# Kernel tuning notes

Measured on AMD Instinct MI355X. Metric: run time of the kernel, lower is better.

## Reference

```python
import jax, jax.numpy as jnp
import numpy as np

B, Y = 1024, 50000
MAX_TRIALS = 4096


def setup_inputs() -> dict:
    key = jax.random.key(0)
    k1, k2 = jax.random.split(key)
    input_ = jax.random.normal(k1, (B, Y), dtype=jnp.float32)
    pos = jax.random.randint(k2, (B,), 0, Y)
    target = jnp.zeros((B, Y), jnp.float32).at[jnp.arange(B), pos].set(1.0)
    return {"input_": input_, "target": target, "max_num_trials": MAX_TRIALS}


def reference(input_, target, max_num_trials):
    """WARP loss. The torch original sequentially samples negatives WITHOUT
    replacement per row until margin 1 + s_neg - s_pos >= 0 or max_num_trials
    is hit. Sampling without replacement == taking a uniform random
    permutation of the negative labels and scanning it; the first violating
    position t gives num_trials = t+1. This lets us fully vectorize the
    irregular loop while computing identical math (up to RNG stream)."""
    Bn, Yn = input_.shape
    rows = jnp.arange(Bn)
    pos = jnp.argmax(target, axis=1)                 # one positive per row (as J[i,1])
    pos_score = input_[rows, pos]                    # [B]

    # uniform random permutation of the Y-1 negatives per row:
    # random sort keys, force the positive label to sort last, drop it.
    u = jax.random.uniform(jax.random.key(42), (Bn, Yn))
    u = u.at[rows, pos].set(2.0)
    perm = jnp.argsort(u, axis=1)[:, : Yn - 1]       # [B, Y-1] negative label ids

    neg_scores = jnp.take_along_axis(input_, perm, axis=1)   # [B, Y-1]
    margins = 1.0 + neg_scores - pos_score[:, None]
    trial_ok = jnp.arange(Yn - 1)[None, :] < max_num_trials
    viol = (margins >= 0.0) & trial_ok
    found = jnp.any(viol, axis=1)
    first = jnp.argmax(viol, axis=1)                 # first violating trial index
    num_trials = (first + 1).astype(jnp.float32)
    # loss_weight = log(floor((Y-1)/num_trials)); 0 when no violator found
    L = jnp.where(found, jnp.log(jnp.floor((Yn - 1.0) / num_trials)), 0.0)
    neg_score = jnp.where(
        found, jnp.take_along_axis(neg_scores, first[:, None], axis=1)[:, 0], 0.0
    )
    loss = L * (1.0 - pos_score + neg_score)         # [B]
    return jnp.sum(loss, keepdims=True)              # shape (1,), as torch.sum(dim=0, keepdim=True)
```

## Files before the change

### kernel.cpp

```cpp
#include <hip/hip_runtime.h>
#include <stdint.h>

#define BN 1024
#define YN 50000
#define SEGS 8
#define SEGLEN 6250
#define CAP 192
#define KEYHI_T (1u << 14)

#define TF_ROUND(r) { x0 += x1; x1 = (x1 << (r)) | (x1 >> (32 - (r))); x1 ^= x0; }

__device__ __forceinline__ uint32_t tf_bits(uint32_t ctr) {
    const uint32_t ks0 = 0u;
    const uint32_t ks1 = 42u;
    const uint32_t ks2 = 0x1BD11BDAu ^ 0u ^ 42u;
    uint32_t x0 = ks0;
    uint32_t x1 = ctr + ks1;
    TF_ROUND(13) TF_ROUND(15) TF_ROUND(26) TF_ROUND(6)
    x0 += ks1; x1 += ks2 + 1u;
    TF_ROUND(17) TF_ROUND(29) TF_ROUND(16) TF_ROUND(24)
    x0 += ks2; x1 += ks0 + 2u;
    TF_ROUND(13) TF_ROUND(15) TF_ROUND(26) TF_ROUND(6)
    x0 += ks0; x1 += ks1 + 3u;
    TF_ROUND(17) TF_ROUND(29) TF_ROUND(16) TF_ROUND(24)
    x0 += ks1; x1 += ks2 + 4u;
    TF_ROUND(13) TF_ROUND(15) TF_ROUND(26) TF_ROUND(6)
    x0 += ks2; x1 += ks0 + 5u;
    return x0 ^ x1;
}

struct WS {
    uint32_t* cnt; int* flag; int* pos; float* ps; float* row_loss; uint32_t* cand;
};
static inline WS ws_layout(void* d_ws) {
    uint32_t* p = (uint32_t*)d_ws;
    WS w;
    w.cnt = p; w.flag = (int*)(p + BN); w.pos = (int*)(p + 2 * BN);
    w.ps = (float*)(p + 3 * BN); w.row_loss = (float*)(p + 4 * BN);
    w.cand = p + 5 * BN;
    return w;
}

__global__ __launch_bounds__(256) void gen_kernel(
    const float* __restrict__ input, const float* __restrict__ target,
    uint32_t* __restrict__ cnt, uint32_t* __restrict__ cand,
    int* __restrict__ pos_out, float* __restrict__ ps_out)
{
    const int tid = threadIdx.x;
    if (blockIdx.x < BN) {
        const int row = blockIdx.x;
        const size_t base = (size_t)row * YN;
        __shared__ volatile int s_pos;
        if (tid == 0) s_pos = -1;
        __syncthreads();
        const float4* t4 = (const float4*)(target + base);
        for (int j4 = tid; j4 < YN / 4; j4 += 256) {
            if (s_pos >= 0) break;
            float4 v = t4[j4];
            int c0 = 4 * j4;
            if (v.x != 0.0f) s_pos = c0;
            if (v.y != 0.0f) s_pos = c0 + 1;
            if (v.z != 0.0f) s_pos = c0 + 2;
            if (v.w != 0.0f) s_pos = c0 + 3;
        }
        __syncthreads();
        if (tid == 0) {
            int p = s_pos;
            pos_out[row] = p;
            ps_out[row] = input[base + p];
        }
        return;
    }
    const int b = blockIdx.x - BN;
    const int row = b >> 3;
    const int seg = b & 7;
    const uint32_t base32 = (uint32_t)row * YN;
    const int start = seg * SEGLEN;
    const int end = start + SEGLEN;
    uint32_t* mycnt = cnt + row;
    uint32_t* mycand = cand + row * CAP;
    for (int col = start + tid; col < end; col += 256) {
        uint32_t bits = tf_bits(base32 + (uint32_t)col);
        uint32_t kh = bits >> 9;
        if (kh < KEYHI_T) {
            uint32_t idx = atomicAdd(mycnt, 1u);
            if (idx < CAP) mycand[idx] = (kh << 17) | (uint32_t)col;
        }
    }
}

__global__ __launch_bounds__(256) void resolve_kernel(
    const float* __restrict__ input, const uint32_t* __restrict__ cnt,
    const uint32_t* __restrict__ cand, const int* __restrict__ pos_,
    const float* __restrict__ ps_, const int* __restrict__ mt_ptr,
    float* __restrict__ row_loss, int* __restrict__ flag)
{
    const int gtid = blockIdx.x * 256 + threadIdx.x;
    const int row = gtid >> 6;
    const int lane = gtid & 63;
    const uint32_t n = cnt[row];
    if (n > CAP) { if (lane == 0) flag[row] = 1; return; }
    const int pos = pos_[row];
    const float ps = ps_[row];
    const uint32_t* cl = cand + row * CAP;
    const float* rowp = input + (size_t)row * YN;

    uint32_t mk = 0xFFFFFFFFu;
    for (uint32_t i = lane; i < n; i += 64) {
        uint32_t e = cl[i];
        int col = (int)(e & 0x1FFFFu);
        if (col == pos) continue;
        float s = rowp[col];
        if ((1.0f + s) - ps >= 0.0f) mk = (e < mk) ? e : mk;
    }
    for (int off = 32; off > 0; off >>= 1) {
        uint32_t o = (uint32_t)__shfl_xor((int)mk, off, 64);
        mk = (o < mk) ? o : mk;
    }
    if (mk == 0xFFFFFFFFu) {
        if (lane == 0) flag[row] = 1;
        return;
    }
    uint32_t c = 0;
    for (uint32_t i = lane; i < n; i += 64) {
        uint32_t e = cl[i];
        int col = (int)(e & 0x1FFFFu);
        c += ((e < mk) && (col != pos)) ? 1u : 0u;
    }
    for (int off = 32; off > 0; off >>= 1) c += (uint32_t)__shfl_xor((int)c, off, 64);
    if (lane == 0) {
        uint32_t rank = c;
        float loss = 0.0f;
        if (rank < (uint32_t)mt_ptr[0]) {
            int cstar = (int)(mk & 0x1FFFFu);
            float ns = rowp[cstar];
            float nt = (float)(rank + 1u);
            loss = logf(floorf(49999.0f / nt)) * ((1.0f - ps) + ns);
        }
        row_loss[row] = loss;
    }
}

__global__ __launch_bounds__(256) void fallback_kernel(
    const float* __restrict__ input, const int* __restrict__ flag,
    const int* __restrict__ pos_, const float* __restrict__ ps_,
    const int* __restrict__ mt_ptr, float* __restrict__ row_loss)
{
    const int row = blockIdx.x;
    if (!flag[row]) return;
    const int tid = threadIdx.x;
    const int pos = pos_[row];
    const float ps = ps_[row];
    const uint32_t base32 = (uint32_t)row * YN;
    const float* rowp = input + (size_t)row * YN;

    __shared__ uint64_t smin[256];
    __shared__ uint32_t ssum[256];

    uint64_t mk = ~0ull;
    for (int col = tid; col < YN; col += 256) {
        uint32_t bits = tf_bits(base32 + (uint32_t)col);
        uint64_t key = ((uint64_t)(bits >> 9) << 17) | (uint32_t)col;
        float m = (1.0f + rowp[col]) - ps;
        if ((m >= 0.0f) && (col != pos) && (key < mk)) mk = key;
    }
    smin[tid] = mk;
    __syncthreads();
    for (int s = 128; s > 0; s >>= 1) {
        if (tid < s) { uint64_t o = smin[tid + s]; if (o < smin[tid]) smin[tid] = o; }
        __syncthreads();
    }
    const uint64_t kstar = smin[0];
    if (kstar == ~0ull) {
        if (tid == 0) row_loss[row] = 0.0f;
        return;
    }
    uint32_t c = 0;
    for (int col = tid; col < YN; col += 256) {
        uint32_t bits = tf_bits(base32 + (uint32_t)col);
        uint64_t key = ((uint64_t)(bits >> 9) << 17) | (uint32_t)col;
        c += ((key < kstar) && (col != pos)) ? 1u : 0u;
    }
    ssum[tid] = c;
    __syncthreads();
    for (int s = 128; s > 0; s >>= 1) {
        if (tid < s) ssum[tid] += ssum[tid + s];
        __syncthreads();
    }
    if (tid == 0) {
        uint32_t rank = ssum[0];
        float loss = 0.0f;
        if (rank < (uint32_t)mt_ptr[0]) {
            int cstar = (int)(kstar & 0x1FFFFull);
            float ns = rowp[cstar];
            float nt = (float)(rank + 1u);
            loss = logf(floorf(49999.0f / nt)) * ((1.0f - ps) + ns);
        }
        row_loss[row] = loss;
    }
}

__global__ __launch_bounds__(256) void reduce_kernel(
    const float* __restrict__ row_loss, float* __restrict__ out)
{
    __shared__ float s[256];
    int tid = threadIdx.x;
    float acc = 0.0f;
    for (int i = tid; i < BN; i += 256) acc += row_loss[i];
    s[tid] = acc;
    __syncthreads();
    for (int st = 128; st > 0; st >>= 1) {
        if (tid < st) s[tid] += s[tid + st];
        __syncthreads();
    }
    if (tid == 0) out[0] = s[0];
}

extern "C" void kernel_launch(void* const* d_in, const int* in_sizes, int n_in,
                              void* d_out, int out_size, void* d_ws, size_t ws_size,
                              hipStream_t stream) {
    const float* input  = (const float*)d_in[0];
    const float* target = (const float*)d_in[1];
    const int*   mt     = (const int*)d_in[2];
    float* out = (float*)d_out;
    WS w = ws_layout(d_ws);

    hipMemsetAsync(d_ws, 0, 2 * BN * sizeof(uint32_t), stream);

    gen_kernel<<<BN + BN * SEGS, 256, 0, stream>>>(
        input, target, w.cnt, w.cand, w.pos, w.ps);
    resolve_kernel<<<BN / 4, 256, 0, stream>>>(
        input, w.cnt, w.cand, w.pos, w.ps, mt, w.row_loss, w.flag);
    fallback_kernel<<<BN, 256, 0, stream>>>(
        input, w.flag, w.pos, w.ps, mt, w.row_loss);
    reduce_kernel<<<1, 256, 0, stream>>>(w.row_loss, out);
}
```

Before: 457.0 us.

## Use per-segment LDS candidate counters, 4-wide Threefry, lower key threshold

Candidate collection now counts in shared memory per segment block and writes one per-segment count, so the global atomics and the workspace memset go away. Threefry is computed four counters at a time using the alignbit rotate, which adds instruction-level parallelism. The key threshold is halved so each segment holds at most 32 candidates, and resolve reads a fixed 256 slots held in registers. The risk is that more rows find no violator among the smaller candidate set or overflow a segment, which sends them to the expensive fallback scan.

```diff
diff --git a/kernel.cpp b/kernel.cpp
--- a/kernel.cpp
+++ b/kernel.cpp
@@ -5,45 +5,73 @@
 #define YN 50000
 #define SEGS 8
 #define SEGLEN 6250
-#define CAP 192
-#define KEYHI_T (1u << 14)
-
-#define TF_ROUND(r) { x0 += x1; x1 = (x1 << (r)) | (x1 >> (32 - (r))); x1 ^= x0; }
+#define SEGCAP 32
+#define KEYHI_T (1u << 13)
+
+#define ROTL(x, r) __builtin_amdgcn_alignbit((x), (x), 32u - (r))
+#define TF4(r) { \
+    x0[0] += x1[0]; x0[1] += x1[1]; x0[2] += x1[2]; x0[3] += x1[3]; \
+    x1[0] = ROTL(x1[0], r); x1[1] = ROTL(x1[1], r); \
+    x1[2] = ROTL(x1[2], r); x1[3] = ROTL(x1[3], r); \
+    x1[0] ^= x0[0]; x1[1] ^= x0[1]; x1[2] ^= x0[2]; x1[3] ^= x0[3]; }
+#define INJ4(a, b) { \
+    x0[0] += (a); x0[1] += (a); x0[2] += (a); x0[3] += (a); \
+    x1[0] += (b); x1[1] += (b); x1[2] += (b); x1[3] += (b); }
+
+__device__ __forceinline__ void tf_bits4(uint32_t ctr0, uint32_t out[4]) {
+    const uint32_t ks0 = 0u, ks1 = 42u, ks2 = 0x1BD11BDAu ^ 0u ^ 42u;
+    uint32_t x0[4], x1[4];
+#pragma unroll
+    for (int k = 0; k < 4; ++k) { x0[k] = ks0; x1[k] = ctr0 + (uint32_t)k + ks1; }
+    TF4(13) TF4(15) TF4(26) TF4(6)
+    INJ4(ks1, ks2 + 1u)
+    TF4(17) TF4(29) TF4(16) TF4(24)
+    INJ4(ks2, ks0 + 2u)
+    TF4(13) TF4(15) TF4(26) TF4(6)
+    INJ4(ks0, ks1 + 3u)
+    TF4(17) TF4(29) TF4(16) TF4(24)
+    INJ4(ks1, ks2 + 4u)
+    TF4(13) TF4(15) TF4(26) TF4(6)
+    INJ4(ks2, ks0 + 5u)
+#pragma unroll
+    for (int k = 0; k < 4; ++k) out[k] = x0[k] ^ x1[k];
+}
 
 __device__ __forceinline__ uint32_t tf_bits(uint32_t ctr) {
-    const uint32_t ks0 = 0u;
-    const uint32_t ks1 = 42u;
-    const uint32_t ks2 = 0x1BD11BDAu ^ 0u ^ 42u;
-    uint32_t x0 = ks0;
-    uint32_t x1 = ctr + ks1;
-    TF_ROUND(13) TF_ROUND(15) TF_ROUND(26) TF_ROUND(6)
+    const uint32_t ks0 = 0u, ks1 = 42u, ks2 = 0x1BD11BDAu ^ 0u ^ 42u;
+    uint32_t x0 = ks0, x1 = ctr + ks1;
+#define TFR(r) { x0 += x1; x1 = ROTL(x1, r); x1 ^= x0; }
+    TFR(13) TFR(15) TFR(26) TFR(6)
     x0 += ks1; x1 += ks2 + 1u;
-    TF_ROUND(17) TF_ROUND(29) TF_ROUND(16) TF_ROUND(24)
+    TFR(17) TFR(29) TFR(16) TFR(24)
     x0 += ks2; x1 += ks0 + 2u;
-    TF_ROUND(13) TF_ROUND(15) TF_ROUND(26) TF_ROUND(6)
+    TFR(13) TFR(15) TFR(26) TFR(6)
     x0 += ks0; x1 += ks1 + 3u;
-    TF_ROUND(17) TF_ROUND(29) TF_ROUND(16) TF_ROUND(24)
+    TFR(17) TFR(29) TFR(16) TFR(24)
     x0 += ks1; x1 += ks2 + 4u;
-    TF_ROUND(13) TF_ROUND(15) TF_ROUND(26) TF_ROUND(6)
+    TFR(13) TFR(15) TFR(26) TFR(6)
     x0 += ks2; x1 += ks0 + 5u;
     return x0 ^ x1;
 }
 
 struct WS {
-    uint32_t* cnt; int* flag; int* pos; float* ps; float* row_loss; uint32_t* cand;
+    uint32_t* cnt_seg; int* pos; float* ps; float* row_loss; int* flag; uint32_t* cand;
 };
 static inline WS ws_layout(void* d_ws) {
     uint32_t* p = (uint32_t*)d_ws;
     WS w;
-    w.cnt = p; w.flag = (int*)(p + BN); w.pos = (int*)(p + 2 * BN);
-    w.ps = (float*)(p + 3 * BN); w.row_loss = (float*)(p + 4 * BN);
-    w.cand = p + 5 * BN;
+    w.cnt_seg = p;
+    w.pos = (int*)(p + SEGS * BN);
+    w.ps = (float*)(p + (SEGS + 1) * BN);
+    w.row_loss = (float*)(p + (SEGS + 2) * BN);
+    w.flag = (int*)(p + (SEGS + 3) * BN);
+    w.cand = p + (SEGS + 4) * BN;
     return w;
 }
 
 __global__ __launch_bounds__(256) void gen_kernel(
     const float* __restrict__ input, const float* __restrict__ target,
-    uint32_t* __restrict__ cnt, uint32_t* __restrict__ cand,
+    uint32_t* __restrict__ cnt_seg, uint32_t* __restrict__ cand,
     int* __restrict__ pos_out, float* __restrict__ ps_out)
 {
     const int tid = threadIdx.x;
@@ -74,23 +102,32 @@
     const int b = blockIdx.x - BN;
     const int row = b >> 3;
     const int seg = b & 7;
-    const uint32_t base32 = (uint32_t)row * YN;
+    const uint32_t rowbase = (uint32_t)row * (uint32_t)YN;
     const int start = seg * SEGLEN;
     const int end = start + SEGLEN;
-    uint32_t* mycnt = cnt + row;
-    uint32_t* mycand = cand + row * CAP;
-    for (int col = start + tid; col < end; col += 256) {
-        uint32_t bits = tf_bits(base32 + (uint32_t)col);
-        uint32_t kh = bits >> 9;
-        if (kh < KEYHI_T) {
-            uint32_t idx = atomicAdd(mycnt, 1u);
-            if (idx < CAP) mycand[idx] = (kh << 17) | (uint32_t)col;
-        }
-    }
+    __shared__ uint32_t lcnt;
+    if (tid == 0) lcnt = 0;
+    __syncthreads();
+    uint32_t* mycand = cand + (size_t)(row * SEGS + seg) * SEGCAP;
+    for (int col0 = start + tid * 4; col0 < end; col0 += 1024) {
+        uint32_t o[4];
+        tf_bits4(rowbase + (uint32_t)col0, o);
+#pragma unroll
+        for (int k = 0; k < 4; ++k) {
+            uint32_t kh = o[k] >> 9;
+            int col = col0 + k;
+            if (kh < KEYHI_T && col < end) {
+                uint32_t idx = atomicAdd(&lcnt, 1u);
+                if (idx < SEGCAP) mycand[idx] = (kh << 17) | (uint32_t)col;
+            }
+        }
+    }
+    __syncthreads();
+    if (tid == 0) cnt_seg[row * SEGS + seg] = lcnt;
 }
 
 __global__ __launch_bounds__(256) void resolve_kernel(
-    const float* __restrict__ input, const uint32_t* __restrict__ cnt,
+    const float* __restrict__ input, const uint32_t* __restrict__ cnt_seg,
     const uint32_t* __restrict__ cand, const int* __restrict__ pos_,
     const float* __restrict__ ps_, const int* __restrict__ mt_ptr,
     float* __restrict__ row_loss, int* __restrict__ flag)
@@ -98,20 +135,34 @@
     const int gtid = blockIdx.x * 256 + threadIdx.x;
     const int row = gtid >> 6;
     const int lane = gtid & 63;
-    const uint32_t n = cnt[row];
-    if (n > CAP) { if (lane == 0) flag[row] = 1; return; }
+    const uint32_t* cs = cnt_seg + row * SEGS;
+    uint32_t csl[SEGS];
+    bool over = false;
+#pragma unroll
+    for (int s = 0; s < SEGS; ++s) { csl[s] = cs[s]; over |= (csl[s] > SEGCAP); }
+    if (over) { if (lane == 0) flag[row] = 1; return; }
+
     const int pos = pos_[row];
     const float ps = ps_[row];
-    const uint32_t* cl = cand + row * CAP;
+    const uint32_t* cl = cand + (size_t)row * SEGS * SEGCAP;
     const float* rowp = input + (size_t)row * YN;
 
+    uint32_t ecache[4]; bool vcache[4];
     uint32_t mk = 0xFFFFFFFFu;
-    for (uint32_t i = lane; i < n; i += 64) {
-        uint32_t e = cl[i];
-        int col = (int)(e & 0x1FFFFu);
-        if (col == pos) continue;
-        float s = rowp[col];
-        if ((1.0f + s) - ps >= 0.0f) mk = (e < mk) ? e : mk;
+#pragma unroll
+    for (int it = 0; it < 4; ++it) {
+        int slot = lane + 64 * it;
+        int s = slot >> 5, idx = slot & 31;
+        bool valid = (uint32_t)idx < csl[s];
+        uint32_t e = valid ? cl[slot] : 0xFFFFFFFFu;
+        ecache[it] = e; vcache[it] = valid;
+        if (valid) {
+            int col = (int)(e & 0x1FFFFu);
+            if (col != pos) {
+                float sc = rowp[col];
+                if ((1.0f + sc) - ps >= 0.0f && e < mk) mk = e;
+            }
+        }
     }
     for (int off = 32; off > 0; off >>= 1) {
         uint32_t o = (uint32_t)__shfl_xor((int)mk, off, 64);
@@ -122,13 +173,15 @@
         return;
     }
     uint32_t c = 0;
-    for (uint32_t i = lane; i < n; i += 64) {
-        uint32_t e = cl[i];
+#pragma unroll
+    for (int it = 0; it < 4; ++it) {
+        uint32_t e = ecache[it];
         int col = (int)(e & 0x1FFFFu);
-        c += ((e < mk) && (col != pos)) ? 1u : 0u;
+        c += (vcache[it] && (e < mk) && (col != pos)) ? 1u : 0u;
     }
     for (int off = 32; off > 0; off >>= 1) c += (uint32_t)__shfl_xor((int)c, off, 64);
     if (lane == 0) {
+        flag[row] = 0;
         uint32_t rank = c;
         float loss = 0.0f;
         if (rank < (uint32_t)mt_ptr[0]) {
@@ -151,7 +204,7 @@
     const int tid = threadIdx.x;
     const int pos = pos_[row];
     const float ps = ps_[row];
-    const uint32_t base32 = (uint32_t)row * YN;
+    const uint32_t base32 = (uint32_t)row * (uint32_t)YN;
     const float* rowp = input + (size_t)row * YN;
 
     __shared__ uint64_t smin[256];
@@ -225,12 +278,10 @@
     float* out = (float*)d_out;
     WS w = ws_layout(d_ws);
 
-    hipMemsetAsync(d_ws, 0, 2 * BN * sizeof(uint32_t), stream);
-
     gen_kernel<<<BN + BN * SEGS, 256, 0, stream>>>(
-        input, target, w.cnt, w.cand, w.pos, w.ps);
+        input, target, w.cnt_seg, w.cand, w.pos, w.ps);
     resolve_kernel<<<BN / 4, 256, 0, stream>>>(
-        input, w.cnt, w.cand, w.pos, w.ps, mt, w.row_loss, w.flag);
+        input, w.cnt_seg, w.cand, w.pos, w.ps, mt, w.row_loss, w.flag);
     fallback_kernel<<<BN, 256, 0, stream>>>(
         input, w.flag, w.pos, w.ps, mt, w.row_loss);
     reduce_kernel<<<1, 256, 0, stream>>>(w.row_loss, out);
```

Result: slower. 548.2 us (+20.0%).

## Interleave four Threefry hashes per thread over flattened index space

Applied to the files above, without the earlier changes.

The candidate generation pass now walks the flattened B*Y counter space with a grid-stride loop. Each thread evaluates four Threefry streams interleaved, using alignbit rotates, and folds the zero key-schedule additions away. The candidate threshold and capacity are halved, and the resolve kernel loads at most two candidates per lane without loops and clears the fallback flag itself, so the memset shrinks. This aims to cut ALU and issue cost in the hash-dominated pass. In exchange it computes per-element row/col by division, and the smaller candidate set slightly raises the chance of the slow fallback path.

```diff
diff --git a/kernel.cpp b/kernel.cpp
--- a/kernel.cpp
+++ b/kernel.cpp
@@ -3,45 +3,49 @@
 
 #define BN 1024
 #define YN 50000
-#define SEGS 8
-#define SEGLEN 6250
-#define CAP 192
-#define KEYHI_T (1u << 14)
-
-#define TF_ROUND(r) { x0 += x1; x1 = (x1 << (r)) | (x1 >> (32 - (r))); x1 ^= x0; }
+#define NTOT (BN * YN)
+#define NGROUPS (NTOT / 4)
+#define CAP 96
+#define BITS_T (1u << 22)
+#define HASH_BLOCKS 4096
+#define STRIDE (HASH_BLOCKS * 256)
+
+#define ROTL(x, r) __builtin_amdgcn_alignbit((x), (x), 32u - (r))
+#define RND(b, a, r) { b += a; a = ROTL(a, r); a ^= b; }
+#define RND4(r) { RND(b0,a0,r) RND(b1,a1,r) RND(b2,a2,r) RND(b3,a3,r) }
+#define INJ4(db, da) { b0 += (db); b1 += (db); b2 += (db); b3 += (db); \
+                       a0 += (da); a1 += (da); a2 += (da); a3 += (da); }
 
 __device__ __forceinline__ uint32_t tf_bits(uint32_t ctr) {
-    const uint32_t ks0 = 0u;
-    const uint32_t ks1 = 42u;
-    const uint32_t ks2 = 0x1BD11BDAu ^ 0u ^ 42u;
-    uint32_t x0 = ks0;
-    uint32_t x1 = ctr + ks1;
-    TF_ROUND(13) TF_ROUND(15) TF_ROUND(26) TF_ROUND(6)
+    const uint32_t ks1 = 42u, ks2 = 0x1BD11BF0u;
+    uint32_t x0 = 0u, x1 = ctr + ks1;
+#define TFR(r) { x0 += x1; x1 = ROTL(x1, r); x1 ^= x0; }
+    TFR(13) TFR(15) TFR(26) TFR(6)
     x0 += ks1; x1 += ks2 + 1u;
-    TF_ROUND(17) TF_ROUND(29) TF_ROUND(16) TF_ROUND(24)
-    x0 += ks2; x1 += ks0 + 2u;
-    TF_ROUND(13) TF_ROUND(15) TF_ROUND(26) TF_ROUND(6)
-    x0 += ks0; x1 += ks1 + 3u;
-    TF_ROUND(17) TF_ROUND(29) TF_ROUND(16) TF_ROUND(24)
+    TFR(17) TFR(29) TFR(16) TFR(24)
+    x0 += ks2; x1 += 2u;
+    TFR(13) TFR(15) TFR(26) TFR(6)
+    x1 += ks1 + 3u;
+    TFR(17) TFR(29) TFR(16) TFR(24)
     x0 += ks1; x1 += ks2 + 4u;
-    TF_ROUND(13) TF_ROUND(15) TF_ROUND(26) TF_ROUND(6)
-    x0 += ks2; x1 += ks0 + 5u;
+    TFR(13) TFR(15) TFR(26) TFR(6)
+    x0 += ks2; x1 += 5u;
     return x0 ^ x1;
 }
 
 struct WS {
-    uint32_t* cnt; int* flag; int* pos; float* ps; float* row_loss; uint32_t* cand;
+    uint32_t* cnt; int* pos; float* ps; float* row_loss; int* flag; uint32_t* cand;
 };
 static inline WS ws_layout(void* d_ws) {
     uint32_t* p = (uint32_t*)d_ws;
     WS w;
-    w.cnt = p; w.flag = (int*)(p + BN); w.pos = (int*)(p + 2 * BN);
-    w.ps = (float*)(p + 3 * BN); w.row_loss = (float*)(p + 4 * BN);
+    w.cnt = p; w.pos = (int*)(p + BN); w.ps = (float*)(p + 2 * BN);
+    w.row_loss = (float*)(p + 3 * BN); w.flag = (int*)(p + 4 * BN);
     w.cand = p + 5 * BN;
     return w;
 }
 
-__global__ __launch_bounds__(256) void gen_kernel(
+__global__ __launch_bounds__(256, 4) void gen_kernel(
     const float* __restrict__ input, const float* __restrict__ target,
     uint32_t* __restrict__ cnt, uint32_t* __restrict__ cand,
     int* __restrict__ pos_out, float* __restrict__ ps_out)
@@ -71,20 +75,39 @@
         }
         return;
     }
-    const int b = blockIdx.x - BN;
-    const int row = b >> 3;
-    const int seg = b & 7;
-    const uint32_t base32 = (uint32_t)row * YN;
-    const int start = seg * SEGLEN;
-    const int end = start + SEGLEN;
-    uint32_t* mycnt = cnt + row;
-    uint32_t* mycand = cand + row * CAP;
-    for (int col = start + tid; col < end; col += 256) {
-        uint32_t bits = tf_bits(base32 + (uint32_t)col);
-        uint32_t kh = bits >> 9;
-        if (kh < KEYHI_T) {
-            uint32_t idx = atomicAdd(mycnt, 1u);
-            if (idx < CAP) mycand[idx] = (kh << 17) | (uint32_t)col;
+    const uint32_t gid = (uint32_t)(blockIdx.x - BN) * 256u + (uint32_t)tid;
+    const uint32_t ks1 = 42u, ks2 = 0x1BD11BF0u;
+    for (uint32_t g = gid; g < NGROUPS; g += STRIDE) {
+        const uint32_t c4 = g << 2;
+        uint32_t a0 = c4 + 42u, a1 = c4 + 43u, a2 = c4 + 44u, a3 = c4 + 45u;
+        uint32_t b0 = 0u, b1 = 0u, b2 = 0u, b3 = 0u;
+        RND4(13) RND4(15) RND4(26) RND4(6)
+        INJ4(ks1, ks2 + 1u)
+        RND4(17) RND4(29) RND4(16) RND4(24)
+        INJ4(ks2, 2u)
+        RND4(13) RND4(15) RND4(26) RND4(6)
+        INJ4(0u, ks1 + 3u)
+        RND4(17) RND4(29) RND4(16) RND4(24)
+        INJ4(ks1, ks2 + 4u)
+        RND4(13) RND4(15) RND4(26) RND4(6)
+        INJ4(ks2, 5u)
+        const uint32_t o0 = b0 ^ a0, o1 = b1 ^ a1, o2 = b2 ^ a2, o3 = b3 ^ a3;
+        const uint32_t m01 = o0 < o1 ? o0 : o1;
+        const uint32_t m23 = o2 < o3 ? o2 : o3;
+        const uint32_t m = m01 < m23 ? m01 : m23;
+        if (__builtin_expect(m < BITS_T, 0)) {
+            const uint32_t os[4] = {o0, o1, o2, o3};
+#pragma unroll
+            for (int k = 0; k < 4; ++k) {
+                if (os[k] < BITS_T) {
+                    const uint32_t idx = c4 + (uint32_t)k;
+                    const uint32_t row = idx / 50000u;
+                    const uint32_t col = idx - row * 50000u;
+                    const uint32_t slot = atomicAdd(&cnt[row], 1u);
+                    if (slot < CAP)
+                        cand[row * CAP + slot] = ((os[k] >> 9) << 17) | col;
+                }
+            }
         }
     }
 }
@@ -105,13 +128,18 @@
     const uint32_t* cl = cand + row * CAP;
     const float* rowp = input + (size_t)row * YN;
 
+    uint32_t e0 = 0xFFFFFFFFu, e1 = 0xFFFFFFFFu;
+    if ((uint32_t)lane < n) e0 = cl[lane];
+    if ((uint32_t)(lane + 64) < n) e1 = cl[lane + 64];
+
     uint32_t mk = 0xFFFFFFFFu;
-    for (uint32_t i = lane; i < n; i += 64) {
-        uint32_t e = cl[i];
-        int col = (int)(e & 0x1FFFFu);
-        if (col == pos) continue;
-        float s = rowp[col];
-        if ((1.0f + s) - ps >= 0.0f) mk = (e < mk) ? e : mk;
+    {
+        int col = (int)(e0 & 0x1FFFFu);
+        if (e0 != 0xFFFFFFFFu && col != pos &&
+            (1.0f + rowp[col]) - ps >= 0.0f) mk = e0;
+        col = (int)(e1 & 0x1FFFFu);
+        if (e1 != 0xFFFFFFFFu && col != pos &&
+            (1.0f + rowp[col]) - ps >= 0.0f && e1 < mk) mk = e1;
     }
     for (int off = 32; off > 0; off >>= 1) {
         uint32_t o = (uint32_t)__shfl_xor((int)mk, off, 64);
@@ -122,19 +150,16 @@
         return;
     }
     uint32_t c = 0;
-    for (uint32_t i = lane; i < n; i += 64) {
-        uint32_t e = cl[i];
-        int col = (int)(e & 0x1FFFFu);
-        c += ((e < mk) && (col != pos)) ? 1u : 0u;
-    }
+    c += (e0 < mk && (int)(e0 & 0x1FFFFu) != pos) ? 1u : 0u;
+    c += (e1 < mk && (int)(e1 & 0x1FFFFu) != pos) ? 1u : 0u;
     for (int off = 32; off > 0; off >>= 1) c += (uint32_t)__shfl_xor((int)c, off, 64);
     if (lane == 0) {
-        uint32_t rank = c;
+        flag[row] = 0;
         float loss = 0.0f;
-        if (rank < (uint32_t)mt_ptr[0]) {
+        if (c < (uint32_t)mt_ptr[0]) {
             int cstar = (int)(mk & 0x1FFFFu);
             float ns = rowp[cstar];
-            float nt = (float)(rank + 1u);
+            float nt = (float)(c + 1u);
             loss = logf(floorf(49999.0f / nt)) * ((1.0f - ps) + ns);
         }
         row_loss[row] = loss;
@@ -151,7 +176,7 @@
     const int tid = threadIdx.x;
     const int pos = pos_[row];
     const float ps = ps_[row];
-    const uint32_t base32 = (uint32_t)row * YN;
+    const uint32_t base32 = (uint32_t)row * (uint32_t)YN;
     const float* rowp = input + (size_t)row * YN;
 
     __shared__ uint64_t smin[256];
@@ -161,8 +186,8 @@
     for (int col = tid; col < YN; col += 256) {
         uint32_t bits = tf_bits(base32 + (uint32_t)col);
         uint64_t key = ((uint64_t)(bits >> 9) << 17) | (uint32_t)col;
-        float m = (1.0f + rowp[col]) - ps;
-        if ((m >= 0.0f) && (col != pos) && (key < mk)) mk = key;
+        float mrg = (1.0f + rowp[col]) - ps;
+        if ((mrg >= 0.0f) && (col != pos) && (key < mk)) mk = key;
     }
     smin[tid] = mk;
     __syncthreads();
@@ -225,9 +250,8 @@
     float* out = (float*)d_out;
     WS w = ws_layout(d_ws);
 
-    hipMemsetAsync(d_ws, 0, 2 * BN * sizeof(uint32_t), stream);
-
-    gen_kernel<<<BN + BN * SEGS, 256, 0, stream>>>(
+    hipMemsetAsync(w.cnt, 0, BN * sizeof(uint32_t), stream);
+    gen_kernel<<<BN + HASH_BLOCKS, 256, 0, stream>>>(
         input, target, w.cnt, w.cand, w.pos, w.ps);
     resolve_kernel<<<BN / 4, 256, 0, stream>>>(
         input, w.cnt, w.cand, w.pos, w.ps, mt, w.row_loss, w.flag);
```

Result: slower. 541.7 us (+18.5%).
